# Optimization experiments

Measured on AMD Instinct MI355X. Metric: run time of the kernel, lower is better.

## Reference

```python
import jax, jax.numpy as jnp
import numpy as np


def _conv1x1(x, w, b):
    # x: [B, Cin, H, W], w: [Cout, Cin], b: [Cout]
    return jnp.einsum('bchw,oc->bohw', x, w) + b[None, :, None, None]


def setup_inputs() -> dict:
    key = jax.random.key(0)
    ks = jax.random.split(key, 9)
    B, C, H, W = 32, 512, 32, 32
    Cout, dn = 512, 512
    s_in = 1.0 / np.sqrt(C)
    s_out = 1.0 / np.sqrt(Cout)
    return {
        'x': jax.random.normal(ks[0], (B, C, H, W), jnp.float32),
        'wA': jax.random.uniform(ks[1], (Cout, C), jnp.float32, -s_in, s_in),
        'bA': jax.random.uniform(ks[2], (Cout,), jnp.float32, -s_in, s_in),
        'wB': jax.random.uniform(ks[3], (dn, C), jnp.float32, -s_in, s_in),
        'bB': jax.random.uniform(ks[4], (dn,), jnp.float32, -s_in, s_in),
        'wV': jax.random.uniform(ks[5], (dn, C), jnp.float32, -s_in, s_in),
        'bV': jax.random.uniform(ks[6], (dn,), jnp.float32, -s_in, s_in),
        'wR': jax.random.uniform(ks[7], (Cout, Cout), jnp.float32, -s_out, s_out),
        'bR': jax.random.uniform(ks[8], (Cout,), jnp.float32, -s_out, s_out),
    }


def reference(x, wA, bA, wB, bB, wV, bV, wR, bR):
    Bsz, C, H, W = x.shape
    Cout = wA.shape[0]
    A = _conv1x1(x, wA, bA).reshape(Bsz, Cout, H * W)          # [B, Cout, N]
    Bm = _conv1x1(x, wB, bB).reshape(Bsz, wB.shape[0], H * W)  # [B, dn, N]
    Vm = _conv1x1(x, wV, bV).reshape(Bsz, wV.shape[0], H * W)  # [B, dn, N]
    attn_maps = jax.nn.softmax(Bm, axis=-1)                    # softmax over spatial
    attn_vectors = jax.nn.softmax(Vm, axis=-1)                 # softmax over spatial
    glob_desc = jnp.einsum('bcn,bdn->bcd', A, attn_maps)       # [B, Cout, dn]
    Z = jnp.einsum('bcd,bdn->bcn', glob_desc, attn_vectors)    # [B, Cout, N]
    Z = Z.reshape(Bsz, Cout, H, W)
    Z = _conv1x1(Z, wR, bR)
    return Z
```

## Files before the change

### kernel.cpp

```cpp
#include <hip/hip_runtime.h>
#include <stdint.h>

typedef unsigned short u16;
typedef __bf16  bf16x8 __attribute__((ext_vector_type(8)));
typedef float   f32x4  __attribute__((ext_vector_type(4)));

__device__ __forceinline__ u16 f2bf(float f) {
    union { float f; unsigned u; } c; c.f = f;
    unsigned r = c.u + 0x7fffu + ((c.u >> 16) & 1u);
    return (u16)(r >> 16);
}
__device__ __forceinline__ float bf2f(u16 b) {
    union { unsigned u; float f; } c; c.u = ((unsigned)b) << 16; return c.f;
}

__device__ __forceinline__ void g2l16(const u16* g, u16* l) {
    __builtin_amdgcn_global_load_lds(
        (__attribute__((address_space(1))) void*)(uintptr_t)g,
        (__attribute__((address_space(3))) void*)(uint32_t)(uintptr_t)l,
        16, 0, 0);
}

template <bool HAS_BIAS, bool OUT_F32>
__global__ __launch_bounds__(256) void gemm_nt(
    const u16* __restrict__ A, const u16* __restrict__ B, void* __restrict__ C,
    const float* __restrict__ bias, int M, int N, int K,
    long sA, long sB, long sC)
{
    __shared__ __align__(16) u16 As[128 * 64];
    __shared__ __align__(16) u16 Bs[128 * 64];

    const int bz = blockIdx.z;
    const int m0 = blockIdx.y * 128;
    const int n0 = blockIdx.x * 128;
    const u16* Ab = A + (long)bz * sA;
    const u16* Bb = B + (long)bz * sB;

    const int t = threadIdx.x;
    const int w = t >> 6, lane = t & 63;
    const int wr = w >> 1, wc = w & 1;

    f32x4 acc[4][4];
    const f32x4 zero = {0.f, 0.f, 0.f, 0.f};
#pragma unroll
    for (int i = 0; i < 4; ++i)
#pragma unroll
        for (int j = 0; j < 4; ++j) acc[i][j] = zero;

    int  sOff[4];
    long aoff[4], boff[4];
#pragma unroll
    for (int i = 0; i < 4; ++i) {
        const int s   = i * 256 + w * 64 + lane;
        const int row = s >> 3;
        const int col = ((s & 7) ^ (row & 7)) * 8;
        sOff[i] = s * 8;
        aoff[i] = (long)(m0 + row) * K + col;
        boff[i] = (long)(n0 + row) * K + col;
    }

    const int fr = lane & 15;
    const int q  = lane >> 4;
    const int o0 = ((q ^ (fr & 7)) * 8);
    const u16* fa = &As[(wr * 64 + fr) * 64];
    const u16* fb = &Bs[(wc * 64 + fr) * 64];

    for (int k0 = 0; k0 < K; k0 += 64) {
#pragma unroll
        for (int i = 0; i < 4; ++i) g2l16(Ab + aoff[i] + k0, &As[sOff[i]]);
#pragma unroll
        for (int i = 0; i < 4; ++i) g2l16(Bb + boff[i] + k0, &Bs[sOff[i]]);
        __syncthreads();

#pragma unroll
        for (int kh = 0; kh < 2; ++kh) {
            const int o = o0 ^ (kh * 32);
            bf16x8 af[4], bv[4];
#pragma unroll
            for (int mi = 0; mi < 4; ++mi) af[mi] = *(const bf16x8*)(fa + mi * 1024 + o);
#pragma unroll
            for (int ni = 0; ni < 4; ++ni) bv[ni] = *(const bf16x8*)(fb + ni * 1024 + o);
#pragma unroll
            for (int mi = 0; mi < 4; ++mi)
#pragma unroll
                for (int ni = 0; ni < 4; ++ni)
                    acc[mi][ni] = __builtin_amdgcn_mfma_f32_16x16x32_bf16(
                        af[mi], bv[ni], acc[mi][ni], 0, 0, 0);
        }
        __syncthreads();
    }

    const int ccol  = n0 + wc * 64 + fr;
    const int crow0 = m0 + wr * 64 + (lane >> 4) * 4;
#pragma unroll
    for (int mi = 0; mi < 4; ++mi) {
#pragma unroll
        for (int r = 0; r < 4; ++r) {
            const int row = crow0 + mi * 16 + r;
            float bvs = HAS_BIAS ? bias[row] : 0.f;
#pragma unroll
            for (int ni = 0; ni < 4; ++ni) {
                const float v = acc[mi][ni][r] + bvs;
                const long idx = (long)bz * sC + (long)row * N + ccol + ni * 16;
                if (OUT_F32) ((float*)C)[idx] = v;
                else         ((u16*)C)[idx]   = f2bf(v);
            }
        }
    }
}

__global__ __launch_bounds__(256) void cast_transpose_x(
    const float* __restrict__ in, u16* __restrict__ out)
{
    __shared__ u16 tile[64][65];
    const int bz = blockIdx.z;
    const float* ip = in  + (long)bz * (512 * 1024);
    u16*         op = out + (long)bz * (1024 * 512);
    const int c0 = blockIdx.x * 64;
    const int r0 = blockIdx.y * 64;
    const int tx = threadIdx.x;
    const int ty = threadIdx.y;
#pragma unroll
    for (int i = ty; i < 64; i += 4)
        tile[i][tx] = f2bf(ip[(long)(r0 + i) * 1024 + c0 + tx]);
    __syncthreads();
#pragma unroll
    for (int i = ty; i < 64; i += 4)
        op[(long)(c0 + i) * 512 + r0 + tx] = tile[tx][i];
}

__global__ __launch_bounds__(256) void transpose_rc(
    const u16* __restrict__ in, u16* __restrict__ out, long sIn, long sOut)
{
    __shared__ u16 tile[64][65];
    const int bz = blockIdx.z;
    const u16* ip = in  + (long)bz * sIn;
    u16*       op = out + (long)bz * sOut;
    const int c0 = blockIdx.x * 64;
    const int r0 = blockIdx.y * 64;
    const int tx = threadIdx.x;
    const int ty = threadIdx.y;
#pragma unroll
    for (int i = ty; i < 64; i += 4)
        tile[i][tx] = ip[(long)(r0 + i) * 1024 + c0 + tx];
    __syncthreads();
#pragma unroll
    for (int i = ty; i < 64; i += 4)
        op[(long)(c0 + i) * 512 + r0 + tx] = tile[tx][i];
}

__global__ __launch_bounds__(256) void cast_weights(
    const float* __restrict__ wA, const float* __restrict__ wB,
    const float* __restrict__ wV, const float* __restrict__ wR,
    const float* __restrict__ bA, const float* __restrict__ bB,
    const float* __restrict__ bV,
    u16* __restrict__ Wcat, u16* __restrict__ wRb, float* __restrict__ bcat)
{
    const int tid = blockIdx.x * 256 + threadIdx.x;
    if (tid < 786432) {
        const int wsel = tid >> 18, off = tid & 262143;
        const float* src = (wsel == 0) ? wA : (wsel == 1) ? wB : wV;
        Wcat[tid] = f2bf(src[off]);
    } else if (tid < 1048576) {
        wRb[tid - 786432] = f2bf(wR[tid - 786432]);
    } else if (tid < 1048576 + 1536) {
        const int j = tid - 1048576;
        bcat[j] = (j < 512) ? bA[j] : (j < 1024) ? bB[j - 512] : bV[j - 1024];
    }
}

__global__ __launch_bounds__(256) void softmax_rows(u16* __restrict__ Y)
{
    u16* row = Y + (long)blockIdx.y * (1536 * 1024) + (long)(512 + blockIdx.x) * 1024;
    const int t = threadIdx.x;
    ushort4 u = ((const ushort4*)row)[t];
    float v0 = bf2f(u.x), v1 = bf2f(u.y), v2 = bf2f(u.z), v3 = bf2f(u.w);

    float m = fmaxf(fmaxf(v0, v1), fmaxf(v2, v3));
#pragma unroll
    for (int off = 32; off > 0; off >>= 1) m = fmaxf(m, __shfl_down(m, off));

    __shared__ float smax[4];
    __shared__ float ssum[4];
    const int w = t >> 6, lane = t & 63;
    if (lane == 0) smax[w] = m;
    __syncthreads();
    m = fmaxf(fmaxf(smax[0], smax[1]), fmaxf(smax[2], smax[3]));

    float e0 = __expf(v0 - m), e1 = __expf(v1 - m);
    float e2 = __expf(v2 - m), e3 = __expf(v3 - m);
    float s = e0 + e1 + e2 + e3;
#pragma unroll
    for (int off = 32; off > 0; off >>= 1) s += __shfl_down(s, off);
    if (lane == 0) ssum[w] = s;
    __syncthreads();
    const float inv = 1.0f / (ssum[0] + ssum[1] + ssum[2] + ssum[3]);

    ushort4 o;
    o.x = f2bf(e0 * inv); o.y = f2bf(e1 * inv);
    o.z = f2bf(e2 * inv); o.w = f2bf(e3 * inv);
    ((ushort4*)row)[t] = o;
}

extern "C" void kernel_launch(void* const* d_in, const int* in_sizes, int n_in,
                              void* d_out, int out_size, void* d_ws, size_t ws_size,
                              hipStream_t stream)
{
    (void)in_sizes; (void)n_in; (void)out_size; (void)ws_size;
    const float* x  = (const float*)d_in[0];
    const float* wA = (const float*)d_in[1];
    const float* bA = (const float*)d_in[2];
    const float* wB = (const float*)d_in[3];
    const float* bB = (const float*)d_in[4];
    const float* wV = (const float*)d_in[5];
    const float* bV = (const float*)d_in[6];
    const float* wR = (const float*)d_in[7];
    const float* bR = (const float*)d_in[8];
    float* out = (float*)d_out;

    const int B = 32;
    const long sY = (long)1536 * 1024;

    char* p = (char*)d_ws;
    u16*   Y    = (u16*)p;   p += (long)B * sY * 2;
    u16*   Gt   = (u16*)p;   p += (long)B * 512 * 512 * 2;
    u16*   Wcat = (u16*)p;   p += (long)1536 * 512 * 2;
    u16*   wRb  = (u16*)p;   p += (long)512 * 512 * 2;
    float* bcat = (float*)p; p += 1536 * 4;

    u16* Xt = (u16*)d_out;
    u16* Vt = Y;
    u16* G2 = Y + (long)512 * 1024;

    cast_transpose_x<<<dim3(16, 8, B), dim3(64, 4), 0, stream>>>(x, Xt);
    cast_weights<<<dim3(4103), 256, 0, stream>>>(wA, wB, wV, wR, bA, bB, bV,
                                                 Wcat, wRb, bcat);

    gemm_nt<true, false><<<dim3(8, 12, B), 256, 0, stream>>>(
        Wcat, Xt, Y, bcat, 1536, 1024, 512, 0, (long)1024 * 512, sY);

    softmax_rows<<<dim3(1024, B), 256, 0, stream>>>(Y);

    gemm_nt<false, false><<<dim3(4, 4, B), 256, 0, stream>>>(
        Y + (long)512 * 1024, Y, Gt, nullptr, 512, 512, 1024,
        sY, sY, (long)512 * 512);

    transpose_rc<<<dim3(16, 8, B), dim3(64, 4), 0, stream>>>(
        Y + (long)1024 * 1024, Vt, sY, sY);

    gemm_nt<false, false><<<dim3(4, 4, B), 256, 0, stream>>>(
        wRb, Gt, G2, nullptr, 512, 512, 512, 0, (long)512 * 512, sY);

    gemm_nt<true, true><<<dim3(8, 4, B), 256, 0, stream>>>(
        G2, Vt, out, bR, 512, 1024, 512, sY, sY, (long)512 * 1024);
}
```

Measured before the change: 330.5 us.

## Template GEMM M-tile to 64 for smaller GEMMs and vectorize transposes

The GEMM kernel now takes the M tile height as a template parameter. The three smaller GEMMs use 64-row tiles, which doubles their block count, gives better CU coverage on this GPU, and cuts per-thread accumulator registers. The price is less data reuse per block. The cast-transpose and transpose kernels are rewritten to use 1D blocks with 4-wide vector global loads and stores, and the shared tile padding changes to match. This is meant to reduce the number of memory transactions in those bandwidth-bound passes.

Result: no change. 335.1 us (+1.4%).

```diff
diff --git a/kernel.cpp b/kernel.cpp
--- a/kernel.cpp
+++ b/kernel.cpp
@@ -21,17 +21,19 @@
         16, 0, 0);
 }
 
-template <bool HAS_BIAS, bool OUT_F32>
+template <int TM, bool HAS_BIAS, bool OUT_F32>
 __global__ __launch_bounds__(256) void gemm_nt(
     const u16* __restrict__ A, const u16* __restrict__ B, void* __restrict__ C,
     const float* __restrict__ bias, int M, int N, int K,
     long sA, long sB, long sC)
 {
-    __shared__ __align__(16) u16 As[128 * 64];
+    constexpr int MI = TM / 32;
+    constexpr int NA = TM / 32;
+    __shared__ __align__(16) u16 As[TM * 64];
     __shared__ __align__(16) u16 Bs[128 * 64];
 
     const int bz = blockIdx.z;
-    const int m0 = blockIdx.y * 128;
+    const int m0 = blockIdx.y * TM;
     const int n0 = blockIdx.x * 128;
     const u16* Ab = A + (long)bz * sA;
     const u16* Bb = B + (long)bz * sB;
@@ -40,48 +42,55 @@
     const int w = t >> 6, lane = t & 63;
     const int wr = w >> 1, wc = w & 1;
 
-    f32x4 acc[4][4];
+    f32x4 acc[MI][4];
     const f32x4 zero = {0.f, 0.f, 0.f, 0.f};
 #pragma unroll
-    for (int i = 0; i < 4; ++i)
+    for (int i = 0; i < MI; ++i)
 #pragma unroll
         for (int j = 0; j < 4; ++j) acc[i][j] = zero;
 
-    int  sOff[4];
-    long aoff[4], boff[4];
-#pragma unroll
-    for (int i = 0; i < 4; ++i) {
-        const int s   = i * 256 + w * 64 + lane;
+    int  aslot[NA]; long aoff[NA];
+#pragma unroll
+    for (int i = 0; i < NA; ++i) {
+        const int s   = i * 256 + t;
         const int row = s >> 3;
         const int col = ((s & 7) ^ (row & 7)) * 8;
-        sOff[i] = s * 8;
-        aoff[i] = (long)(m0 + row) * K + col;
-        boff[i] = (long)(n0 + row) * K + col;
+        aslot[i] = s * 8;
+        aoff[i]  = (long)(m0 + row) * K + col;
+    }
+    int  bslot[4]; long boff[4];
+#pragma unroll
+    for (int i = 0; i < 4; ++i) {
+        const int s   = i * 256 + t;
+        const int row = s >> 3;
+        const int col = ((s & 7) ^ (row & 7)) * 8;
+        bslot[i] = s * 8;
+        boff[i]  = (long)(n0 + row) * K + col;
     }
 
     const int fr = lane & 15;
     const int q  = lane >> 4;
     const int o0 = ((q ^ (fr & 7)) * 8);
-    const u16* fa = &As[(wr * 64 + fr) * 64];
+    const u16* fa = &As[(wr * (TM / 2) + fr) * 64];
     const u16* fb = &Bs[(wc * 64 + fr) * 64];
 
     for (int k0 = 0; k0 < K; k0 += 64) {
 #pragma unroll
-        for (int i = 0; i < 4; ++i) g2l16(Ab + aoff[i] + k0, &As[sOff[i]]);
-#pragma unroll
-        for (int i = 0; i < 4; ++i) g2l16(Bb + boff[i] + k0, &Bs[sOff[i]]);
+        for (int i = 0; i < NA; ++i) g2l16(Ab + aoff[i] + k0, &As[aslot[i]]);
+#pragma unroll
+        for (int i = 0; i < 4; ++i)  g2l16(Bb + boff[i] + k0, &Bs[bslot[i]]);
         __syncthreads();
 
 #pragma unroll
         for (int kh = 0; kh < 2; ++kh) {
             const int o = o0 ^ (kh * 32);
-            bf16x8 af[4], bv[4];
-#pragma unroll
-            for (int mi = 0; mi < 4; ++mi) af[mi] = *(const bf16x8*)(fa + mi * 1024 + o);
-#pragma unroll
-            for (int ni = 0; ni < 4; ++ni) bv[ni] = *(const bf16x8*)(fb + ni * 1024 + o);
-#pragma unroll
-            for (int mi = 0; mi < 4; ++mi)
+            bf16x8 af[MI], bv[4];
+#pragma unroll
+            for (int mi = 0; mi < MI; ++mi) af[mi] = *(const bf16x8*)(fa + mi * 1024 + o);
+#pragma unroll
+            for (int ni = 0; ni < 4; ++ni)  bv[ni] = *(const bf16x8*)(fb + ni * 1024 + o);
+#pragma unroll
+            for (int mi = 0; mi < MI; ++mi)
 #pragma unroll
                 for (int ni = 0; ni < 4; ++ni)
                     acc[mi][ni] = __builtin_amdgcn_mfma_f32_16x16x32_bf16(
@@ -91,9 +100,9 @@
     }
 
     const int ccol  = n0 + wc * 64 + fr;
-    const int crow0 = m0 + wr * 64 + (lane >> 4) * 4;
-#pragma unroll
-    for (int mi = 0; mi < 4; ++mi) {
+    const int crow0 = m0 + wr * (TM / 2) + (lane >> 4) * 4;
+#pragma unroll
+    for (int mi = 0; mi < MI; ++mi) {
 #pragma unroll
         for (int r = 0; r < 4; ++r) {
             const int row = crow0 + mi * 16 + r;
@@ -112,41 +121,63 @@
 __global__ __launch_bounds__(256) void cast_transpose_x(
     const float* __restrict__ in, u16* __restrict__ out)
 {
-    __shared__ u16 tile[64][65];
+    __shared__ u16 tile[64][68];
     const int bz = blockIdx.z;
     const float* ip = in  + (long)bz * (512 * 1024);
     u16*         op = out + (long)bz * (1024 * 512);
     const int c0 = blockIdx.x * 64;
     const int r0 = blockIdx.y * 64;
-    const int tx = threadIdx.x;
-    const int ty = threadIdx.y;
-#pragma unroll
-    for (int i = ty; i < 64; i += 4)
-        tile[i][tx] = f2bf(ip[(long)(r0 + i) * 1024 + c0 + tx]);
-    __syncthreads();
-#pragma unroll
-    for (int i = ty; i < 64; i += 4)
-        op[(long)(c0 + i) * 512 + r0 + tx] = tile[tx][i];
+    const int tx = threadIdx.x & 15;
+    const int ty = threadIdx.x >> 4;
+#pragma unroll
+    for (int p = 0; p < 4; ++p) {
+        const int row = ty + 16 * p;
+        float4 v = *(const float4*)(ip + (long)(r0 + row) * 1024 + c0 + 4 * tx);
+        ushort4 o;
+        o.x = f2bf(v.x); o.y = f2bf(v.y); o.z = f2bf(v.z); o.w = f2bf(v.w);
+        *(ushort4*)&tile[row][4 * tx] = o;
+    }
+    __syncthreads();
+#pragma unroll
+    for (int p = 0; p < 4; ++p) {
+        const int orow = ty + 16 * p;
+        ushort4 o;
+        o.x = tile[4 * tx + 0][orow];
+        o.y = tile[4 * tx + 1][orow];
+        o.z = tile[4 * tx + 2][orow];
+        o.w = tile[4 * tx + 3][orow];
+        *(ushort4*)&op[(long)(c0 + orow) * 512 + r0 + 4 * tx] = o;
+    }
 }
 
 __global__ __launch_bounds__(256) void transpose_rc(
     const u16* __restrict__ in, u16* __restrict__ out, long sIn, long sOut)
 {
-    __shared__ u16 tile[64][65];
+    __shared__ u16 tile[64][68];
     const int bz = blockIdx.z;
     const u16* ip = in  + (long)bz * sIn;
     u16*       op = out + (long)bz * sOut;
     const int c0 = blockIdx.x * 64;
     const int r0 = blockIdx.y * 64;
-    const int tx = threadIdx.x;
-    const int ty = threadIdx.y;
-#pragma unroll
-    for (int i = ty; i < 64; i += 4)
-        tile[i][tx] = ip[(long)(r0 + i) * 1024 + c0 + tx];
-    __syncthreads();
-#pragma unroll
-    for (int i = ty; i < 64; i += 4)
-        op[(long)(c0 + i) * 512 + r0 + tx] = tile[tx][i];
+    const int tx = threadIdx.x & 15;
+    const int ty = threadIdx.x >> 4;
+#pragma unroll
+    for (int p = 0; p < 4; ++p) {
+        const int row = ty + 16 * p;
+        ushort4 v = *(const ushort4*)(ip + (long)(r0 + row) * 1024 + c0 + 4 * tx);
+        *(ushort4*)&tile[row][4 * tx] = v;
+    }
+    __syncthreads();
+#pragma unroll
+    for (int p = 0; p < 4; ++p) {
+        const int orow = ty + 16 * p;
+        ushort4 o;
+        o.x = tile[4 * tx + 0][orow];
+        o.y = tile[4 * tx + 1][orow];
+        o.z = tile[4 * tx + 2][orow];
+        o.w = tile[4 * tx + 3][orow];
+        *(ushort4*)&op[(long)(c0 + orow) * 512 + r0 + 4 * tx] = o;
+    }
 }
 
 __global__ __launch_bounds__(256) void cast_weights(
@@ -232,25 +263,25 @@
     u16* Vt = Y;
     u16* G2 = Y + (long)512 * 1024;
 
-    cast_transpose_x<<<dim3(16, 8, B), dim3(64, 4), 0, stream>>>(x, Xt);
+    cast_transpose_x<<<dim3(16, 8, B), 256, 0, stream>>>(x, Xt);
     cast_weights<<<dim3(4103), 256, 0, stream>>>(wA, wB, wV, wR, bA, bB, bV,
                                                  Wcat, wRb, bcat);
 
-    gemm_nt<true, false><<<dim3(8, 12, B), 256, 0, stream>>>(
+    gemm_nt<128, true, false><<<dim3(8, 12, B), 256, 0, stream>>>(
         Wcat, Xt, Y, bcat, 1536, 1024, 512, 0, (long)1024 * 512, sY);
 
     softmax_rows<<<dim3(1024, B), 256, 0, stream>>>(Y);
 
-    gemm_nt<false, false><<<dim3(4, 4, B), 256, 0, stream>>>(
+    gemm_nt<64, false, false><<<dim3(4, 8, B), 256, 0, stream>>>(
         Y + (long)512 * 1024, Y, Gt, nullptr, 512, 512, 1024,
         sY, sY, (long)512 * 512);
 
-    transpose_rc<<<dim3(16, 8, B), dim3(64, 4), 0, stream>>>(
+    transpose_rc<<<dim3(16, 8, B), 256, 0, stream>>>(
         Y + (long)1024 * 1024, Vt, sY, sY);
 
-    gemm_nt<false, false><<<dim3(4, 4, B), 256, 0, stream>>>(
+    gemm_nt<64, false, false><<<dim3(4, 8, B), 256, 0, stream>>>(
         wRb, Gt, G2, nullptr, 512, 512, 512, 0, (long)512 * 512, sY);
 
-    gemm_nt<true, true><<<dim3(8, 4, B), 256, 0, stream>>>(
+    gemm_nt<64, true, true><<<dim3(8, 8, B), 256, 0, stream>>>(
         G2, Vt, out, bR, 512, 1024, 512, sY, sY, (long)512 * 1024);
 }
```
